# Performance work log

Hardware: AMD Instinct MI355X
Metric: run time of the kernel (lower is better)

The kernel has to match this reference:

```python
import jax, jax.numpy as jnp
import numpy as np

B, C, H, W = 8, 256, 128, 128
BN_EPS = 1e-5

def setup_inputs() -> dict:
    key = jax.random.key(0)
    ks = jax.random.split(key, 7)
    scale = 1.0 / np.sqrt(C)
    x = jax.random.normal(ks[0], (B, C, H, W), dtype=jnp.float32)
    w_qkv = jax.random.normal(ks[1], (3 * C, C), dtype=jnp.float32) * scale
    w_proj = jax.random.normal(ks[2], (C, C), dtype=jnp.float32) * scale
    gamma = jax.random.uniform(ks[3], (C,), dtype=jnp.float32)
    beta = jax.random.normal(ks[4], (C,), dtype=jnp.float32)
    running_mean = jax.random.normal(ks[5], (C,), dtype=jnp.float32)
    running_var = jax.random.uniform(ks[6], (C,), dtype=jnp.float32) + 0.5
    return {"x": x, "w_qkv": w_qkv, "w_proj": w_proj, "gamma": gamma,
            "beta": beta, "running_mean": running_mean, "running_var": running_var}

def reference(x, w_qkv, w_proj, gamma, beta, running_mean, running_var):
    b, c, h, w = x.shape
    n = h * w
    xf = x.reshape(b, c, n)                       # flatten spatial
    # 1x1 conv == channel matmul: [3c,c] x [b,c,n] -> [b,3c,n]
    qkv = jnp.einsum('oc,bcn->bon', w_qkv, xf)
    q, k, v = jnp.split(qkv, 3, axis=1)           # each [b,c,n]
    k = jax.nn.softmax(k, axis=-1)                # softmax over spatial
    context = jnp.einsum('bcn,bdn->bcd', k, v)    # k @ v^T, [b,c,c]
    out = jnp.einsum('bcd,bcn->bdn', context, q)  # context^T @ q, [b,c,n]
    out = jnp.einsum('oc,bcn->bon', w_proj, out)  # 1x1 proj
    # BatchNorm (inference form with running stats)
    inv = gamma / jnp.sqrt(running_var + BN_EPS)
    out = out * inv[None, :, None] + (beta - running_mean * inv)[None, :, None]
    out = jax.nn.relu(out)
    return out.reshape(b, c, h, w)
```

## Files before the change

### kernel.cpp

```cpp
#include <hip/hip_runtime.h>
#include <stdint.h>

#define B_   8
#define C_   256
#define N_   16384

typedef __attribute__((ext_vector_type(8))) short bf16x8;
typedef __attribute__((ext_vector_type(4))) float f32x4;

__device__ inline unsigned short f2bf(float f) {
    unsigned u = __float_as_uint(f);
    u += 0x7FFF + ((u >> 16) & 1);
    return (unsigned short)(u >> 16);
}

__device__ inline void gl_lds16(const void* g, void* l) {
    __builtin_amdgcn_global_load_lds(
        reinterpret_cast<const __attribute__((address_space(1))) unsigned int*>(
            reinterpret_cast<uintptr_t>(g)),
        reinterpret_cast<__attribute__((address_space(3))) unsigned int*>(
            reinterpret_cast<uintptr_t>(l)),
        16, 0, 0);
}

__device__ inline f32x4 mfma16(bf16x8 a, bf16x8 b, f32x4 c) {
    return __builtin_amdgcn_mfma_f32_16x16x32_bf16(a, b, c, 0, 0, 0);
}

__global__ __launch_bounds__(256) void k1_transpose(const float* __restrict__ x,
                                                    unsigned short* __restrict__ xT) {
    __shared__ unsigned short tile[64][65];
    const int b = blockIdx.z, c0 = blockIdx.y * 64, n0 = blockIdx.x * 64;
    const float* xb = x + (size_t)b * C_ * N_;
    const int t = threadIdx.x;
    const int tr = t >> 4, tc4 = (t & 15) * 4;
#pragma unroll
    for (int p = 0; p < 4; p++) {
        const int i = p * 16 + tr;
        const float4 v = *(const float4*)(xb + (size_t)(c0 + i) * N_ + n0 + tc4);
        tile[i][tc4 + 0] = f2bf(v.x);
        tile[i][tc4 + 1] = f2bf(v.y);
        tile[i][tc4 + 2] = f2bf(v.z);
        tile[i][tc4 + 3] = f2bf(v.w);
    }
    __syncthreads();
    unsigned short* xTb = xT + (size_t)b * N_ * C_;
#pragma unroll
    for (int p = 0; p < 4; p++) {
        const int jj = p * 16 + tr;
        ushort4 o;
        o.x = tile[tc4 + 0][jj];
        o.y = tile[tc4 + 1][jj];
        o.z = tile[tc4 + 2][jj];
        o.w = tile[tc4 + 3][jj];
        *(ushort4*)(xTb + (size_t)(n0 + jj) * C_ + c0 + tc4) = o;
    }
}

__global__ __launch_bounds__(256) void k1b_setup(const float* __restrict__ wqkv,
                                                 const float* __restrict__ gamma,
                                                 const float* __restrict__ beta,
                                                 const float* __restrict__ rmean,
                                                 const float* __restrict__ rvar,
                                                 unsigned short* __restrict__ WkvF,
                                                 float* __restrict__ inv,
                                                 float* __restrict__ b2) {
    const int t = threadIdx.x;
    if (blockIdx.x < 64) {
        const int chunk = blockIdx.x * 256 + t;
        const int lane = chunk & 63;
        const int kb = (chunk >> 6) & 7;
        const int rb = chunk >> 9;
        const int row = rb * 16 + (lane & 15);
        const int k0 = kb * 32 + (lane >> 4) * 8;
        const float* src = wqkv + (size_t)(256 + row) * 256 + k0;
        const float4 a = *(const float4*)(src);
        const float4 c = *(const float4*)(src + 4);
        ushort4 o0, o1;
        o0.x = f2bf(a.x); o0.y = f2bf(a.y); o0.z = f2bf(a.z); o0.w = f2bf(a.w);
        o1.x = f2bf(c.x); o1.y = f2bf(c.y); o1.z = f2bf(c.z); o1.w = f2bf(c.w);
        *(ushort4*)(WkvF + (size_t)chunk * 8) = o0;
        *(ushort4*)(WkvF + (size_t)chunk * 8 + 4) = o1;
    } else {
        const float iv = gamma[t] * rsqrtf(rvar[t] + 1e-5f);
        inv[t] = iv;
        b2[t]  = beta[t] - rmean[t] * iv;
    }
}

__global__ __launch_bounds__(512, 2) void k2_ctx(const unsigned short* __restrict__ WkvF,
                                                 const unsigned short* __restrict__ xT,
                                                 float* __restrict__ cp,
                                                 float* __restrict__ rsum) {
    __shared__ __align__(16) unsigned short xs[2][64 * 256];
    __shared__ __align__(16) unsigned short kvs[384 * 64];
    const int chunk = blockIdx.x;
    const int h  = blockIdx.y;
    const int b  = blockIdx.z;
    const int n0 = chunk * 1024;
    const int t = threadIdx.x, wave = t >> 6, lane = t & 63;
    const int fr = lane & 15, fkq = lane >> 4;
    const int wr = wave >> 1, wc = wave & 1;
    const unsigned short* xTb = xT + (size_t)b * N_ * C_;

    bf16x8 wf[3][8];
    {
        const int rbs[3] = {wave, 8 + wave, 16 + h * 8 + wave};
#pragma unroll
        for (int slot = 0; slot < 3; slot++)
#pragma unroll
            for (int kb = 0; kb < 8; kb++)
                wf[slot][kb] = *(const bf16x8*)(
                    WkvF + (((size_t)rbs[slot] * 8 + kb) * 64 + lane) * 8);
    }

    f32x4 acc[4][4];
#pragma unroll
    for (int i = 0; i < 4; i++)
#pragma unroll
        for (int j = 0; j < 4; j++)
#pragma unroll
            for (int r = 0; r < 4; r++) acc[i][j][r] = 0.f;
    float rsacc[2][4];
#pragma unroll
    for (int i = 0; i < 2; i++)
#pragma unroll
        for (int r = 0; r < 4; r++) rsacc[i][r] = 0.f;

    auto stage = [&](int buf, int sc) {
        const int nb = n0 + sc * 64;
#pragma unroll
        for (int it = 0; it < 4; it++) {
            const int idx = it * 512 + t;
            const int r = idx >> 5;
            const int c = (idx & 31) * 8;
            const int csw = c ^ ((r & 7) * 8);
            gl_lds16(xTb + (size_t)(nb + r) * 256 + csw,
                     &xs[buf][it * 4096 + wave * 512]);
        }
    };

    stage(0, 0);
    __syncthreads();

    for (int s = 0; s < 16; ++s) {
        const int cur = s & 1;
        if (s < 15) stage(cur ^ 1, s + 1);

#pragma unroll 1
        for (int p = 0; p < 2; ++p) {
            f32x4 kacc[3][2];
#pragma unroll
            for (int i = 0; i < 3; i++)
#pragma unroll
                for (int j = 0; j < 2; j++)
#pragma unroll
                    for (int r = 0; r < 4; r++) kacc[i][j][r] = 0.f;
#pragma unroll
            for (int kb = 0; kb < 8; kb++) {
                bf16x8 bfv[2];
#pragma unroll
                for (int jj = 0; jj < 2; jj++) {
                    const int rr = (p * 2 + jj) * 16 + fr;
                    const int cs = (kb * 32 + fkq * 8) ^ ((fr & 7) * 8);
                    bfv[jj] = *(const bf16x8*)(&xs[cur][rr * 256 + cs]);
                }
#pragma unroll
                for (int slot = 0; slot < 3; slot++) {
                    kacc[slot][0] = mfma16(wf[slot][kb], bfv[0], kacc[slot][0]);
                    kacc[slot][1] = mfma16(wf[slot][kb], bfv[1], kacc[slot][1]);
                }
            }
#pragma unroll
            for (int slot = 0; slot < 3; slot++) {
                const int rowb = (slot * 8 + wave) * 16 + fkq * 4;
#pragma unroll
                for (int jj = 0; jj < 2; jj++) {
                    const int cn = (p * 2 + jj) * 16 + fr;
#pragma unroll
                    for (int r = 0; r < 4; r++) {
                        float vv = kacc[slot][jj][r];
                        if (slot < 2) { vv = __expf(vv); rsacc[slot][r] += vv; }
                        const int row = rowb + r;
                        kvs[row * 64 + (cn ^ ((row & 7) * 8))] = f2bf(vv);
                    }
                }
            }
        }
        __syncthreads();

#pragma unroll
        for (int kk = 0; kk < 2; kk++) {
            bf16x8 a2[4], b2v[4];
#pragma unroll
            for (int i = 0; i < 4; i++) {
                const int row = wr * 64 + i * 16 + fr;
                const int cs = (kk * 32 + fkq * 8) ^ ((row & 7) * 8);
                a2[i] = *(const bf16x8*)(&kvs[row * 64 + cs]);
            }
#pragma unroll
            for (int j = 0; j < 4; j++) {
                const int row = 256 + wc * 64 + j * 16 + fr;
                const int cs = (kk * 32 + fkq * 8) ^ ((row & 7) * 8);
                b2v[j] = *(const bf16x8*)(&kvs[row * 64 + cs]);
            }
#pragma unroll
            for (int i = 0; i < 4; i++)
#pragma unroll
                for (int j = 0; j < 4; j++)
                    acc[i][j] = mfma16(a2[i], b2v[j], acc[i][j]);
        }
        __syncthreads();
    }

    float* cpb = cp + ((size_t)((b * 2 + h) * 16 + chunk)) * 256 * 128;
#pragma unroll
    for (int i = 0; i < 4; i++) {
        const int gc = wr * 64 + i * 16 + fkq * 4;
#pragma unroll
        for (int j = 0; j < 4; j++) {
            const int gd = wc * 64 + j * 16 + fr;
#pragma unroll
            for (int r = 0; r < 4; r++)
                cpb[(size_t)(gc + r) * 128 + gd] = acc[i][j][r];
        }
    }
    if (h == 0) {
#pragma unroll
        for (int slot = 0; slot < 2; slot++)
#pragma unroll
            for (int r = 0; r < 4; r++) {
                float sv = rsacc[slot][r];
                sv += __shfl_xor(sv, 1, 64);
                sv += __shfl_xor(sv, 2, 64);
                sv += __shfl_xor(sv, 4, 64);
                sv += __shfl_xor(sv, 8, 64);
                if (fr == 0)
                    atomicAdd(&rsum[b * 256 + (slot * 8 + wave) * 16 + fkq * 4 + r], sv);
            }
    }
}

__global__ __launch_bounds__(256) void k4r_reduce(const float* __restrict__ cp,
                                                  float* __restrict__ ctx) {
    const int gid = blockIdx.x * 256 + threadIdx.x;
    const int d4 = gid & 31;
    const int c  = (gid >> 5) & 255;
    const int h  = (gid >> 13) & 1;
    const int b  = gid >> 14;
    const float* src = cp + ((size_t)((b * 2 + h) * 16) * 256 + c) * 128 + d4 * 4;
    f32x4 s = {0.f, 0.f, 0.f, 0.f};
#pragma unroll
    for (int k = 0; k < 16; k++)
        s = s + *(const f32x4*)(src + (size_t)k * 32768);
    *(f32x4*)(ctx + ((size_t)b * 256 + c) * 256 + h * 128 + d4 * 4) = s;
}

__global__ __launch_bounds__(256) void k5a_T(const float* __restrict__ Wp,
                                             const float* __restrict__ ctx,
                                             const float* __restrict__ rsum,
                                             float* __restrict__ T) {
    __shared__ float Asm[64][65];
    __shared__ float Bsm[64][65];
    const int b = blockIdx.z;
    const int o0 = blockIdx.y * 64, c0 = blockIdx.x * 64;
    const int t = threadIdx.x;
    const int tm = t >> 4, tn = t & 15;
    const int lc4 = tn * 4;
    float acc[4][4] = {};
    const float* cb = ctx + (size_t)b * C_ * C_;
    for (int kk = 0; kk < 256; kk += 64) {
        __syncthreads();
#pragma unroll
        for (int p = 0; p < 4; p++) {
            const int r = p * 16 + tm;
            const float4 av = *(const float4*)(Wp + (size_t)(o0 + r) * C_ + kk + lc4);
            Asm[r][lc4] = av.x; Asm[r][lc4 + 1] = av.y; Asm[r][lc4 + 2] = av.z; Asm[r][lc4 + 3] = av.w;
            const float4 bv = *(const float4*)(cb + (size_t)(c0 + r) * C_ + kk + lc4);
            Bsm[r][lc4] = bv.x; Bsm[r][lc4 + 1] = bv.y; Bsm[r][lc4 + 2] = bv.z; Bsm[r][lc4 + 3] = bv.w;
        }
        __syncthreads();
        for (int k = 0; k < 64; k++) {
            float a_[4], b_[4];
#pragma unroll
            for (int i = 0; i < 4; i++) a_[i] = Asm[tm * 4 + i][k];
#pragma unroll
            for (int j = 0; j < 4; j++) b_[j] = Bsm[tn * 4 + j][k];
#pragma unroll
            for (int i = 0; i < 4; i++)
#pragma unroll
                for (int j = 0; j < 4; j++) acc[i][j] += a_[i] * b_[j];
        }
    }
    float isv[4];
#pragma unroll
    for (int j = 0; j < 4; j++) isv[j] = 1.f / rsum[b * 256 + c0 + tn * 4 + j];
#pragma unroll
    for (int i = 0; i < 4; i++)
#pragma unroll
        for (int j = 0; j < 4; j++)
            T[((size_t)b * C_ + o0 + tm * 4 + i) * C_ + c0 + tn * 4 + j] = acc[i][j] * isv[j];
}

__global__ __launch_bounds__(256) void k5b_G(const float* __restrict__ Tm,
                                             const float* __restrict__ Wq,
                                             const float* __restrict__ inv,
                                             unsigned short* __restrict__ G) {
    __shared__ float Asm[64][65];
    __shared__ float Bsm[64][65];
    const int b = blockIdx.z;
    const int o0 = blockIdx.y * 64, j0 = blockIdx.x * 64;
    const int t = threadIdx.x;
    const int tm = t >> 4, tn = t & 15;
    const int lc4 = tn * 4;
    float acc[4][4] = {};
    const float* Tb = Tm + (size_t)b * C_ * C_;
    for (int kk = 0; kk < 256; kk += 64) {
        __syncthreads();
#pragma unroll
        for (int p = 0; p < 4; p++) {
            const int r = p * 16 + tm;
            const float4 av = *(const float4*)(Tb + (size_t)(o0 + r) * C_ + kk + lc4);
            Asm[r][lc4] = av.x; Asm[r][lc4 + 1] = av.y; Asm[r][lc4 + 2] = av.z; Asm[r][lc4 + 3] = av.w;
            const float4 bv = *(const float4*)(Wq + (size_t)(kk + r) * C_ + j0 + lc4);
            Bsm[r][lc4] = bv.x; Bsm[r][lc4 + 1] = bv.y; Bsm[r][lc4 + 2] = bv.z; Bsm[r][lc4 + 3] = bv.w;
        }
        __syncthreads();
        for (int k = 0; k < 64; k++) {
            float a_[4], b_[4];
#pragma unroll
            for (int i = 0; i < 4; i++) a_[i] = Asm[tm * 4 + i][k];
#pragma unroll
            for (int j = 0; j < 4; j++) b_[j] = Bsm[k][tn * 4 + j];
#pragma unroll
            for (int i = 0; i < 4; i++)
#pragma unroll
                for (int j = 0; j < 4; j++) acc[i][j] += a_[i] * b_[j];
        }
    }
#pragma unroll
    for (int i = 0; i < 4; i++) {
        const float iv = inv[o0 + tm * 4 + i];
#pragma unroll
        for (int j = 0; j < 4; j++)
            G[((size_t)b * C_ + o0 + tm * 4 + i) * C_ + j0 + tn * 4 + j] = f2bf(acc[i][j] * iv);
    }
}

__global__ __launch_bounds__(256) void k6_out(const unsigned short* __restrict__ G,
                                              const unsigned short* __restrict__ xT,
                                              const float* __restrict__ b2,
                                              float* __restrict__ out) {
    __shared__ __align__(16) unsigned short As[128 * 32];
    __shared__ __align__(16) unsigned short Bs[128 * 32];
    const int b  = blockIdx.z;
    const int m0 = blockIdx.y * 128;
    const int n0 = blockIdx.x * 128;
    const int t = threadIdx.x, wave = t >> 6, lane = t & 63;
    const int wm = wave >> 1, wn = wave & 1;

    const unsigned short* Gb  = G  + (size_t)b * C_ * C_;
    const unsigned short* xTb = xT + (size_t)b * N_ * C_;

    const int ch1 = wave * 64 + lane, ch2 = ch1 + 256;
    const int r1 = ch1 >> 2, q1 = ch1 & 3;
    const int r2 = ch2 >> 2, q2 = ch2 & 3;
    unsigned short* ldsA1 = As + wave * 512;
    unsigned short* ldsA2 = As + 2048 + wave * 512;
    unsigned short* ldsB1 = Bs + wave * 512;
    unsigned short* ldsB2 = Bs + 2048 + wave * 512;

    f32x4 acc[4][4];
#pragma unroll
    for (int i = 0; i < 4; i++)
#pragma unroll
        for (int j = 0; j < 4; j++)
#pragma unroll
            for (int r = 0; r < 4; r++) acc[i][j][r] = 0.f;

    const int fr = lane & 15;
    const int fk = (lane >> 4) * 8;

    for (int kk = 0; kk < 256; kk += 32) {
        __syncthreads();
        gl_lds16(Gb  + (size_t)(m0 + r1) * 256 + kk + q1 * 8, ldsA1);
        gl_lds16(Gb  + (size_t)(m0 + r2) * 256 + kk + q2 * 8, ldsA2);
        gl_lds16(xTb + (size_t)(n0 + r1) * 256 + kk + q1 * 8, ldsB1);
        gl_lds16(xTb + (size_t)(n0 + r2) * 256 + kk + q2 * 8, ldsB2);
        __syncthreads();
        bf16x8 af[4], bfv[4];
#pragma unroll
        for (int i = 0; i < 4; i++)
            af[i] = *(const bf16x8*)(As + (wm * 64 + i * 16 + fr) * 32 + fk);
#pragma unroll
        for (int j = 0; j < 4; j++)
            bfv[j] = *(const bf16x8*)(Bs + (wn * 64 + j * 16 + fr) * 32 + fk);
#pragma unroll
        for (int i = 0; i < 4; i++)
#pragma unroll
            for (int j = 0; j < 4; j++)
                acc[i][j] = mfma16(af[i], bfv[j], acc[i][j]);
    }

    const int col = lane & 15, rowq = (lane >> 4) * 4;
    float* ob = out + (size_t)b * C_ * N_;
#pragma unroll
    for (int i = 0; i < 4; i++) {
        const int gm = m0 + wm * 64 + i * 16 + rowq;
#pragma unroll
        for (int j = 0; j < 4; j++) {
            const int gn = n0 + wn * 64 + j * 16 + col;
#pragma unroll
            for (int r = 0; r < 4; r++) {
                const float val = fmaxf(acc[i][j][r] + b2[gm + r], 0.f);
                ob[(size_t)(gm + r) * N_ + gn] = val;
            }
        }
    }
}

extern "C" void kernel_launch(void* const* d_in, const int* in_sizes, int n_in,
                              void* d_out, int out_size, void* d_ws, size_t ws_size,
                              hipStream_t stream) {
    const float* x     = (const float*)d_in[0];
    const float* wqkv  = (const float*)d_in[1];
    const float* wproj = (const float*)d_in[2];
    const float* gamma = (const float*)d_in[3];
    const float* beta  = (const float*)d_in[4];
    const float* rmean = (const float*)d_in[5];
    const float* rvar  = (const float*)d_in[6];
    float* out = (float*)d_out;

    char* ws = (char*)d_ws;
    size_t off = 0;
    auto alloc = [&](size_t bytes) {
        void* p = ws + off;
        off += (bytes + 255) & ~(size_t)255;
        return p;
    };
    unsigned short* xT   = (unsigned short*)alloc((size_t)B_ * N_ * C_ * 2);
    unsigned short* WkvF = (unsigned short*)alloc((size_t)512 * 256 * 2);
    float* invp = (float*)alloc(256 * 4);
    float* b2p  = (float*)alloc(256 * 4);
    float* cp   = (float*)alloc((size_t)256 * 256 * 128 * 4);
    float* ctx  = (float*)alloc((size_t)B_ * C_ * C_ * 4);
    float* rsum = (float*)alloc(2048 * 4);
    float* Tm   = (float*)alloc((size_t)B_ * C_ * C_ * 4);
    unsigned short* G = (unsigned short*)alloc((size_t)B_ * C_ * C_ * 2);

    hipLaunchKernelGGL(k1_transpose, dim3(256, 4, 8), dim3(256), 0, stream, x, xT);
    hipLaunchKernelGGL(k1b_setup, dim3(65), dim3(256), 0, stream,
                       wqkv, gamma, beta, rmean, rvar, WkvF, invp, b2p);
    hipMemsetAsync(rsum, 0, 2048 * 4, stream);
    hipLaunchKernelGGL(k2_ctx, dim3(16, 2, 8), dim3(512), 0, stream, WkvF, xT, cp, rsum);
    hipLaunchKernelGGL(k4r_reduce, dim3(512), dim3(256), 0, stream, cp, ctx);
    hipLaunchKernelGGL(k5a_T, dim3(4, 4, 8), dim3(256), 0, stream, wproj, ctx, rsum, Tm);
    hipLaunchKernelGGL(k5b_G, dim3(4, 4, 8), dim3(256), 0, stream, Tm, wqkv, invp, G);
    hipLaunchKernelGGL(k6_out, dim3(128, 2, 8), dim3(256), 0, stream, G, xT, b2p, out);
}
```

Measured before the change: 384.3 us.

## Halve k2 spatial chunk, double grid, swap MFMA operands for packed kv stores

The context kernel now processes 512 spatial positions per block in 32-row stages, so its grid doubles to 512 blocks. Swapping the MFMA operand order lets each lane hold four consecutive n values, which are packed with v_cvt_pk_bf16 and written as 8-byte stores into a padded (stride 40) kv buffer instead of scattered swizzled 2-byte stores. The rsum zeroing moves into the setup kernel, removing a memset. The cost is twice as many partial context tiles for k4r_reduce to write and sum, plus a larger workspace.

```diff
diff --git a/kernel.cpp b/kernel.cpp
--- a/kernel.cpp
+++ b/kernel.cpp
@@ -5,13 +5,24 @@
 #define C_   256
 #define N_   16384
 
+#define NS    32
+#define KVP   40
+
 typedef __attribute__((ext_vector_type(8))) short bf16x8;
 typedef __attribute__((ext_vector_type(4))) float f32x4;
 
+__device__ inline float bf2f(unsigned short h) {
+    return __uint_as_float(((unsigned)h) << 16);
+}
 __device__ inline unsigned short f2bf(float f) {
     unsigned u = __float_as_uint(f);
     u += 0x7FFF + ((u >> 16) & 1);
     return (unsigned short)(u >> 16);
+}
+__device__ inline unsigned cvt_pk_bf16(float lo, float hi) {
+    unsigned r;
+    asm("v_cvt_pk_bf16_f32 %0, %1, %2" : "=v"(r) : "v"(lo), "v"(hi));
+    return r;
 }
 
 __device__ inline void gl_lds16(const void* g, void* l) {
@@ -64,7 +75,8 @@
                                                  const float* __restrict__ rvar,
                                                  unsigned short* __restrict__ WkvF,
                                                  float* __restrict__ inv,
-                                                 float* __restrict__ b2) {
+                                                 float* __restrict__ b2,
+                                                 float* __restrict__ rsum) {
     const int t = threadIdx.x;
     if (blockIdx.x < 64) {
         const int chunk = blockIdx.x * 256 + t;
@@ -85,6 +97,9 @@
         const float iv = gamma[t] * rsqrtf(rvar[t] + 1e-5f);
         inv[t] = iv;
         b2[t]  = beta[t] - rmean[t] * iv;
+        float4 z = {0.f, 0.f, 0.f, 0.f};
+        *(float4*)(rsum + t * 8)     = z;
+        *(float4*)(rsum + t * 8 + 4) = z;
     }
 }
 
@@ -92,12 +107,12 @@
                                                  const unsigned short* __restrict__ xT,
                                                  float* __restrict__ cp,
                                                  float* __restrict__ rsum) {
-    __shared__ __align__(16) unsigned short xs[2][64 * 256];
-    __shared__ __align__(16) unsigned short kvs[384 * 64];
+    __shared__ __align__(16) unsigned short xs[2][NS * 256];
+    __shared__ __align__(16) unsigned short kvs[384 * KVP];
     const int chunk = blockIdx.x;
     const int h  = blockIdx.y;
     const int b  = blockIdx.z;
-    const int n0 = chunk * 1024;
+    const int n0 = chunk * 512;
     const int t = threadIdx.x, wave = t >> 6, lane = t & 63;
     const int fr = lane & 15, fkq = lane >> 4;
     const int wr = wave >> 1, wc = wave & 1;
@@ -113,6 +128,7 @@
                 wf[slot][kb] = *(const bf16x8*)(
                     WkvF + (((size_t)rbs[slot] * 8 + kb) * 64 + lane) * 8);
     }
+    const int rowbase[3] = {wave * 16, 128 + wave * 16, 256 + wave * 16};
 
     f32x4 acc[4][4];
 #pragma unroll
@@ -121,16 +137,12 @@
         for (int j = 0; j < 4; j++)
 #pragma unroll
             for (int r = 0; r < 4; r++) acc[i][j][r] = 0.f;
-    float rsacc[2][4];
-#pragma unroll
-    for (int i = 0; i < 2; i++)
-#pragma unroll
-        for (int r = 0; r < 4; r++) rsacc[i][r] = 0.f;
+    float rsacc[2] = {0.f, 0.f};
 
     auto stage = [&](int buf, int sc) {
-        const int nb = n0 + sc * 64;
-#pragma unroll
-        for (int it = 0; it < 4; it++) {
+        const int nb = n0 + sc * NS;
+#pragma unroll
+        for (int it = 0; it < 2; it++) {
             const int idx = it * 512 + t;
             const int r = idx >> 5;
             const int c = (idx & 31) * 8;
@@ -147,62 +159,58 @@
         const int cur = s & 1;
         if (s < 15) stage(cur ^ 1, s + 1);
 
-#pragma unroll 1
-        for (int p = 0; p < 2; ++p) {
-            f32x4 kacc[3][2];
-#pragma unroll
-            for (int i = 0; i < 3; i++)
-#pragma unroll
-                for (int j = 0; j < 2; j++)
-#pragma unroll
-                    for (int r = 0; r < 4; r++) kacc[i][j][r] = 0.f;
-#pragma unroll
-            for (int kb = 0; kb < 8; kb++) {
-                bf16x8 bfv[2];
-#pragma unroll
-                for (int jj = 0; jj < 2; jj++) {
-                    const int rr = (p * 2 + jj) * 16 + fr;
-                    const int cs = (kb * 32 + fkq * 8) ^ ((fr & 7) * 8);
-                    bfv[jj] = *(const bf16x8*)(&xs[cur][rr * 256 + cs]);
+        f32x4 kacc[3][2];
+#pragma unroll
+        for (int i = 0; i < 3; i++)
+#pragma unroll
+            for (int j = 0; j < 2; j++)
+#pragma unroll
+                for (int r = 0; r < 4; r++) kacc[i][j][r] = 0.f;
+#pragma unroll
+        for (int kb = 0; kb < 8; kb++) {
+            bf16x8 bfa[2];
+#pragma unroll
+            for (int jj = 0; jj < 2; jj++) {
+                const int rr = jj * 16 + fr;
+                const int cs = (kb * 32 + fkq * 8) ^ ((fr & 7) * 8);
+                bfa[jj] = *(const bf16x8*)(&xs[cur][rr * 256 + cs]);
+            }
+#pragma unroll
+            for (int slot = 0; slot < 3; slot++) {
+                kacc[slot][0] = mfma16(bfa[0], wf[slot][kb], kacc[slot][0]);
+                kacc[slot][1] = mfma16(bfa[1], wf[slot][kb], kacc[slot][1]);
+            }
+        }
+#pragma unroll
+        for (int slot = 0; slot < 3; slot++) {
+            const int kvrow = rowbase[slot] + fr;
+#pragma unroll
+            for (int jj = 0; jj < 2; jj++) {
+                f32x4 v = kacc[slot][jj];
+                if (slot < 2) {
+                    v[0] = __expf(v[0]); v[1] = __expf(v[1]);
+                    v[2] = __expf(v[2]); v[3] = __expf(v[3]);
+                    rsacc[slot] += (v[0] + v[1]) + (v[2] + v[3]);
                 }
-#pragma unroll
-                for (int slot = 0; slot < 3; slot++) {
-                    kacc[slot][0] = mfma16(wf[slot][kb], bfv[0], kacc[slot][0]);
-                    kacc[slot][1] = mfma16(wf[slot][kb], bfv[1], kacc[slot][1]);
-                }
-            }
-#pragma unroll
-            for (int slot = 0; slot < 3; slot++) {
-                const int rowb = (slot * 8 + wave) * 16 + fkq * 4;
-#pragma unroll
-                for (int jj = 0; jj < 2; jj++) {
-                    const int cn = (p * 2 + jj) * 16 + fr;
-#pragma unroll
-                    for (int r = 0; r < 4; r++) {
-                        float vv = kacc[slot][jj][r];
-                        if (slot < 2) { vv = __expf(vv); rsacc[slot][r] += vv; }
-                        const int row = rowb + r;
-                        kvs[row * 64 + (cn ^ ((row & 7) * 8))] = f2bf(vv);
-                    }
-                }
-            }
-        }
-        __syncthreads();
-
-#pragma unroll
-        for (int kk = 0; kk < 2; kk++) {
+                uint2 pk;
+                pk.x = cvt_pk_bf16(v[0], v[1]);
+                pk.y = cvt_pk_bf16(v[2], v[3]);
+                *(uint2*)(&kvs[kvrow * KVP + jj * 16 + fkq * 4]) = pk;
+            }
+        }
+        __syncthreads();
+
+        {
             bf16x8 a2[4], b2v[4];
 #pragma unroll
             for (int i = 0; i < 4; i++) {
                 const int row = wr * 64 + i * 16 + fr;
-                const int cs = (kk * 32 + fkq * 8) ^ ((row & 7) * 8);
-                a2[i] = *(const bf16x8*)(&kvs[row * 64 + cs]);
+                a2[i] = *(const bf16x8*)(&kvs[row * KVP + fkq * 8]);
             }
 #pragma unroll
             for (int j = 0; j < 4; j++) {
                 const int row = 256 + wc * 64 + j * 16 + fr;
-                const int cs = (kk * 32 + fkq * 8) ^ ((row & 7) * 8);
-                b2v[j] = *(const bf16x8*)(&kvs[row * 64 + cs]);
+                b2v[j] = *(const bf16x8*)(&kvs[row * KVP + fkq * 8]);
             }
 #pragma unroll
             for (int i = 0; i < 4; i++)
@@ -213,7 +221,7 @@
         __syncthreads();
     }
 
-    float* cpb = cp + ((size_t)((b * 2 + h) * 16 + chunk)) * 256 * 128;
+    float* cpb = cp + ((size_t)((b * 2 + h) * 32 + chunk)) * 256 * 128;
 #pragma unroll
     for (int i = 0; i < 4; i++) {
         const int gc = wr * 64 + i * 16 + fkq * 4;
@@ -227,17 +235,13 @@
     }
     if (h == 0) {
 #pragma unroll
-        for (int slot = 0; slot < 2; slot++)
-#pragma unroll
-            for (int r = 0; r < 4; r++) {
-                float sv = rsacc[slot][r];
-                sv += __shfl_xor(sv, 1, 64);
-                sv += __shfl_xor(sv, 2, 64);
-                sv += __shfl_xor(sv, 4, 64);
-                sv += __shfl_xor(sv, 8, 64);
-                if (fr == 0)
-                    atomicAdd(&rsum[b * 256 + (slot * 8 + wave) * 16 + fkq * 4 + r], sv);
-            }
+        for (int slot = 0; slot < 2; slot++) {
+            float sv = rsacc[slot];
+            sv += __shfl_xor(sv, 16, 64);
+            sv += __shfl_xor(sv, 32, 64);
+            if (fkq == 0)
+                atomicAdd(&rsum[b * 256 + slot * 128 + wave * 16 + fr], sv);
+        }
     }
 }
 
@@ -248,10 +252,10 @@
     const int c  = (gid >> 5) & 255;
     const int h  = (gid >> 13) & 1;
     const int b  = gid >> 14;
-    const float* src = cp + ((size_t)((b * 2 + h) * 16) * 256 + c) * 128 + d4 * 4;
+    const float* src = cp + ((size_t)((b * 2 + h) * 32) * 256 + c) * 128 + d4 * 4;
     f32x4 s = {0.f, 0.f, 0.f, 0.f};
 #pragma unroll
-    for (int k = 0; k < 16; k++)
+    for (int k = 0; k < 32; k++)
         s = s + *(const f32x4*)(src + (size_t)k * 32768);
     *(f32x4*)(ctx + ((size_t)b * 256 + c) * 256 + h * 128 + d4 * 4) = s;
 }
@@ -442,7 +446,7 @@
     unsigned short* WkvF = (unsigned short*)alloc((size_t)512 * 256 * 2);
     float* invp = (float*)alloc(256 * 4);
     float* b2p  = (float*)alloc(256 * 4);
-    float* cp   = (float*)alloc((size_t)256 * 256 * 128 * 4);
+    float* cp   = (float*)alloc((size_t)512 * 256 * 128 * 4);
     float* ctx  = (float*)alloc((size_t)B_ * C_ * C_ * 4);
     float* rsum = (float*)alloc(2048 * 4);
     float* Tm   = (float*)alloc((size_t)B_ * C_ * C_ * 4);
@@ -450,9 +454,8 @@
 
     hipLaunchKernelGGL(k1_transpose, dim3(256, 4, 8), dim3(256), 0, stream, x, xT);
     hipLaunchKernelGGL(k1b_setup, dim3(65), dim3(256), 0, stream,
-                       wqkv, gamma, beta, rmean, rvar, WkvF, invp, b2p);
-    hipMemsetAsync(rsum, 0, 2048 * 4, stream);
-    hipLaunchKernelGGL(k2_ctx, dim3(16, 2, 8), dim3(512), 0, stream, WkvF, xT, cp, rsum);
+                       wqkv, gamma, beta, rmean, rvar, WkvF, invp, b2p, rsum);
+    hipLaunchKernelGGL(k2_ctx, dim3(32, 2, 8), dim3(512), 0, stream, WkvF, xT, cp, rsum);
     hipLaunchKernelGGL(k4r_reduce, dim3(512), dim3(256), 0, stream, cp, ctx);
     hipLaunchKernelGGL(k5a_T, dim3(4, 4, 8), dim3(256), 0, stream, wproj, ctx, rsum, Tm);
     hipLaunchKernelGGL(k5b_G, dim3(4, 4, 8), dim3(256), 0, stream, Tm, wqkv, invp, G);
```

New measurement: 381.5 us. Within noise of the previous version (-0.7%).
